# Optimization experiments

Measured on AMD Instinct MI355X. Metric: run time of the kernel, lower is better.

Reference implementation:

```python
import jax, jax.numpy as jnp
import numpy as np

B, D, R = 4096, 1024, 256
DT = 0.01
DT_SCALE = 1.0

# Yoshida 4th-order coefficients
_W1 = 1.0 / (2.0 - 2.0 ** (1.0 / 3.0))
_W0 = -(2.0 ** (1.0 / 3.0)) / (2.0 - 2.0 ** (1.0 / 3.0))
C1 = _W1 / 2.0
C2 = (_W0 + _W1) / 2.0
C3 = C2
C4 = C1
D1 = _W1
D2 = _W0
D3 = _W1


def setup_inputs() -> dict:
    key = jax.random.key(0)
    k1, k2, k3, k4, k5 = jax.random.split(key, 5)
    x = jax.random.normal(k1, (B, D), dtype=jnp.float32)
    v = jax.random.normal(k2, (B, D), dtype=jnp.float32)
    force = jax.random.normal(k3, (B, D), dtype=jnp.float32)
    # low-rank christoffel factors, scaled for numerical stability
    U = jax.random.normal(k4, (R, D), dtype=jnp.float32) * (1.0 / np.sqrt(D))
    W = jax.random.normal(k5, (D, R), dtype=jnp.float32) * (1.0 / np.sqrt(R))
    return {"x": x, "v": v, "force": force, "U": U, "W": W}


def _christoffel(tv, tx, U, W):
    # Gamma(v) = W @ (U v)^2  (low-rank quadratic form; x unused, matching
    # the gfn yoshida_fused(U, W) signature)
    h = jnp.einsum("rd,bd->br", U, tv)  # [B, R]
    return jnp.einsum("dr,br->bd", W, h * h)  # [B, D]


def reference(x, v, force, U, W):
    dt = DT * DT_SCALE

    def acceleration(tx, tv):
        return -_christoffel(tv, tx, U, W) + force

    x1 = x + C1 * dt * v
    v1 = v + D1 * dt * acceleration(x1, v)
    x2 = x1 + C2 * dt * v1
    v2 = v1 + D2 * dt * acceleration(x2, v1)
    x3 = x2 + C3 * dt * v2
    v3 = v2 + D3 * dt * acceleration(x3, v2)
    x_final = x3 + C4 * dt * v3
    return (x_final, v3)
```

## Files before the change

### kernel.cpp

```cpp
#include <hip/hip_runtime.h>
#include <hip/hip_bf16.h>


#define BSZ 4096
#define DD 1024
#define RR 256

typedef unsigned short ushort_t;
typedef __attribute__((ext_vector_type(8))) short short8;
typedef __attribute__((ext_vector_type(4))) float f32x4;

__device__ inline ushort_t f2b(float x) {
    union { float f; unsigned int u; } c;
    c.f = x;
    unsigned int lsb = (c.u >> 16) & 1u;
    return (ushort_t)((c.u + 0x7fffu + lsb) >> 16);
}

__global__ __launch_bounds__(256) void pack_uw_kernel(
    const float* __restrict__ U, const float* __restrict__ W,
    ushort_t* __restrict__ Upk, ushort_t* __restrict__ Wpk)
{
    const int g = blockIdx.x * 256 + threadIdx.x;
    if (g < 32768) {
        const int l = g & 63;
        const int kt = (g >> 6) & 31, nt = g >> 11;
        const int r = nt * 16 + (l & 15);
        const int d = kt * 32 + (l >> 4) * 8;
        const float* src = U + (size_t)r * DD + d;
        ushort_t* dst = Upk + (size_t)g * 8;
        #pragma unroll
        for (int j = 0; j < 8; ++j) dst[j] = f2b(src[j]);
    } else {
        const int g2 = g - 32768;
        const int l = g2 & 63;
        const int kt = (g2 >> 6) & 7, dtile = g2 >> 9;
        const int d = dtile * 16 + (l & 15);
        const int r = kt * 32 + (l >> 4) * 8;
        const float* src = W + (size_t)d * RR + r;
        ushort_t* dst = Wpk + (size_t)g2 * 8;
        #pragma unroll
        for (int j = 0; j < 8; ++j) dst[j] = f2b(src[j]);
    }
}

__global__ __launch_bounds__(1024) void yoshida_fused_kernel(
    const float* __restrict__ x_in,
    const float* __restrict__ v_in,
    const float* __restrict__ force,
    const ushort_t* __restrict__ Upk,
    const ushort_t* __restrict__ Wpk,
    float* __restrict__ x_out,
    float* __restrict__ v_out)
{
    __shared__ __align__(16) ushort_t vS[16][1032];
    __shared__ __align__(16) ushort_t H2S[16][264];

    const int tid = threadIdx.x;
    const int w = tid >> 6;
    const int l = tid & 63;
    const int m = l & 15;
    const int q = l >> 4;
    const int b0 = blockIdx.x * 16;
    const int d0 = w * 64;

    constexpr double CBRT2 = 1.2599210498948731647672106072782;
    constexpr double W1c = 1.0 / (2.0 - CBRT2);
    constexpr double W0c = -CBRT2 * W1c;
    constexpr double DTd = 0.01 * 1.0;
    const float dcoef[3] = {(float)(W1c * DTd), (float)(W0c * DTd), (float)(W1c * DTd)};
    const float xcoef[3] = {(float)((W0c + W1c) * 0.5), (float)((W0c + W1c) * 0.5),
                            (float)(W1c * 0.5)};
    const float c1  = (float)(W1c * 0.5);
    const float dtf = (float)DTd;

    {
        const int row = tid >> 6;
        const int col = (tid & 63) * 16;
        const float* src = v_in + (size_t)(b0 + row) * DD + col;
        ushort_t tmp[16];
        #pragma unroll
        for (int j = 0; j < 16; ++j) tmp[j] = f2b(src[j]);
        *(short8*)&vS[row][col]     = *(short8*)&tmp[0];
        *(short8*)&vS[row][col + 8] = *(short8*)&tmp[8];
    }

    float vreg[16], xacc[16];
    #pragma unroll
    for (int t = 0; t < 4; ++t)
        #pragma unroll
        for (int i = 0; i < 4; ++i) {
            const int row = q * 4 + i, col = d0 + t * 16 + m;
            const float vv = v_in[(size_t)(b0 + row) * DD + col];
            vreg[t * 4 + i] = vv;
            xacc[t * 4 + i] = c1 * vv;
        }
    __syncthreads();

    for (int s = 0; s < 3; ++s) {
        f32x4 accA = {0.f, 0.f, 0.f, 0.f};
        const ushort_t* up = Upk + (size_t)(w * 16384 + l * 8);
        #pragma unroll 4
        for (int kt = 0; kt < 32; ++kt) {
            short8 a = *(const short8*)&vS[m][kt * 32 + q * 8];
            short8 b = *(const short8*)(up + (size_t)kt * 512);
            accA = __builtin_amdgcn_mfma_f32_16x16x32_bf16(a, b, accA, 0, 0, 0);
        }
        #pragma unroll
        for (int i = 0; i < 4; ++i) {
            const float h = accA[i];
            H2S[q * 4 + i][w * 16 + m] = f2b(h * h);
        }
        __syncthreads();

        f32x4 accB[4];
        #pragma unroll
        for (int t = 0; t < 4; ++t) accB[t] = (f32x4){0.f, 0.f, 0.f, 0.f};
        const ushort_t* wp = Wpk + (size_t)(w * 16384 + l * 8);
        #pragma unroll 2
        for (int kt = 0; kt < 8; ++kt) {
            short8 a = *(const short8*)&H2S[m][kt * 32 + q * 8];
            #pragma unroll
            for (int t = 0; t < 4; ++t) {
                short8 b = *(const short8*)(wp + (size_t)(t * 8 + kt) * 512);
                accB[t] = __builtin_amdgcn_mfma_f32_16x16x32_bf16(a, b, accB[t], 0, 0, 0);
            }
        }

        const float ddt = dcoef[s], cx = xcoef[s];
        #pragma unroll
        for (int t = 0; t < 4; ++t)
            #pragma unroll
            for (int i = 0; i < 4; ++i) {
                const int row = q * 4 + i, col = d0 + t * 16 + m;
                const float fo = force[(size_t)(b0 + row) * DD + col];
                const float vn = vreg[t * 4 + i] + ddt * (fo - accB[t][i]);
                vreg[t * 4 + i] = vn;
                xacc[t * 4 + i] += cx * vn;
                vS[row][col] = f2b(vn);
            }
        __syncthreads();
    }

    #pragma unroll
    for (int t = 0; t < 4; ++t)
        #pragma unroll
        for (int i = 0; i < 4; ++i) {
            const int row = q * 4 + i, col = d0 + t * 16 + m;
            const size_t g = (size_t)(b0 + row) * DD + col;
            x_out[g] = x_in[g] + dtf * xacc[t * 4 + i];
            v_out[g] = vreg[t * 4 + i];
        }
}

extern "C" void kernel_launch(void* const* d_in, const int* in_sizes, int n_in,
                              void* d_out, int out_size, void* d_ws, size_t ws_size,
                              hipStream_t stream) {
    const float* x     = (const float*)d_in[0];
    const float* v     = (const float*)d_in[1];
    const float* force = (const float*)d_in[2];
    const float* U     = (const float*)d_in[3];
    const float* W     = (const float*)d_in[4];

    float* x_out = (float*)d_out;
    float* v_out = x_out + (size_t)BSZ * DD;

    ushort_t* Upk = (ushort_t*)d_ws;
    ushort_t* Wpk = Upk + (size_t)RR * DD;

    pack_uw_kernel<<<dim3(256), dim3(256), 0, stream>>>(U, W, Upk, Wpk);
    yoshida_fused_kernel<<<dim3(BSZ / 16), dim3(1024), 0, stream>>>(
        x, v, force, Upk, Wpk, x_out, v_out);
}
```

Baseline: 138.0 us.

## Software-pipeline U/W fragment loads, preload force, and vectorize conversions

The U and W bf16 fragments are now prefetched into registers several k-steps ahead in both MFMA loops, the stage loop is fully unrolled, and the first GEMM alternates between two accumulators to shorten the MFMA dependency chain. Force values are loaded once into registers at kernel start instead of being reloaded every stage, and the fp32 loads in the pack kernel and the initial v staging use float4 vector loads. The aim is to hide global-memory latency behind MFMA work and cut redundant traffic, at the cost of higher register pressure in a 1024-thread block.

```diff
diff --git a/kernel.cpp b/kernel.cpp
--- a/kernel.cpp
+++ b/kernel.cpp
@@ -22,26 +22,25 @@
     ushort_t* __restrict__ Upk, ushort_t* __restrict__ Wpk)
 {
     const int g = blockIdx.x * 256 + threadIdx.x;
+    const float* src;
+    ushort_t* dst;
     if (g < 32768) {
         const int l = g & 63;
         const int kt = (g >> 6) & 31, nt = g >> 11;
-        const int r = nt * 16 + (l & 15);
-        const int d = kt * 32 + (l >> 4) * 8;
-        const float* src = U + (size_t)r * DD + d;
-        ushort_t* dst = Upk + (size_t)g * 8;
-        #pragma unroll
-        for (int j = 0; j < 8; ++j) dst[j] = f2b(src[j]);
+        src = U + (size_t)(nt * 16 + (l & 15)) * DD + kt * 32 + (l >> 4) * 8;
+        dst = Upk + (size_t)g * 8;
     } else {
         const int g2 = g - 32768;
         const int l = g2 & 63;
         const int kt = (g2 >> 6) & 7, dtile = g2 >> 9;
-        const int d = dtile * 16 + (l & 15);
-        const int r = kt * 32 + (l >> 4) * 8;
-        const float* src = W + (size_t)d * RR + r;
-        ushort_t* dst = Wpk + (size_t)g2 * 8;
-        #pragma unroll
-        for (int j = 0; j < 8; ++j) dst[j] = f2b(src[j]);
+        src = W + (size_t)(dtile * 16 + (l & 15)) * RR + kt * 32 + (l >> 4) * 8;
+        dst = Wpk + (size_t)g2 * 8;
     }
+    const float4 a = *reinterpret_cast<const float4*>(src);
+    const float4 b = *reinterpret_cast<const float4*>(src + 4);
+    ushort_t t[8] = {f2b(a.x), f2b(a.y), f2b(a.z), f2b(a.w),
+                     f2b(b.x), f2b(b.y), f2b(b.z), f2b(b.w)};
+    *reinterpret_cast<short8*>(dst) = *reinterpret_cast<short8*>(t);
 }
 
 __global__ __launch_bounds__(1024) void yoshida_fused_kernel(
@@ -74,55 +73,79 @@
     const float c1  = (float)(W1c * 0.5);
     const float dtf = (float)DTd;
 
-    {
-        const int row = tid >> 6;
-        const int col = (tid & 63) * 16;
-        const float* src = v_in + (size_t)(b0 + row) * DD + col;
-        ushort_t tmp[16];
-        #pragma unroll
-        for (int j = 0; j < 16; ++j) tmp[j] = f2b(src[j]);
-        *(short8*)&vS[row][col]     = *(short8*)&tmp[0];
-        *(short8*)&vS[row][col + 8] = *(short8*)&tmp[8];
-    }
-
-    float vreg[16], xacc[16];
+    float vreg[16], xacc[16], freg[16];
     #pragma unroll
     for (int t = 0; t < 4; ++t)
         #pragma unroll
         for (int i = 0; i < 4; ++i) {
-            const int row = q * 4 + i, col = d0 + t * 16 + m;
-            const float vv = v_in[(size_t)(b0 + row) * DD + col];
+            const size_t gidx = (size_t)(b0 + q * 4 + i) * DD + d0 + t * 16 + m;
+            const float vv = v_in[gidx];
             vreg[t * 4 + i] = vv;
             xacc[t * 4 + i] = c1 * vv;
+            freg[t * 4 + i] = force[gidx];
         }
-    __syncthreads();
 
+    {
+        const int row = tid >> 6;
+        const int col = (tid & 63) * 16;
+        const float* sp = v_in + (size_t)(b0 + row) * DD + col;
+        const float4 f0 = *reinterpret_cast<const float4*>(sp);
+        const float4 f1 = *reinterpret_cast<const float4*>(sp + 4);
+        const float4 f2 = *reinterpret_cast<const float4*>(sp + 8);
+        const float4 f3 = *reinterpret_cast<const float4*>(sp + 12);
+        ushort_t tmp[16] = {f2b(f0.x), f2b(f0.y), f2b(f0.z), f2b(f0.w),
+                            f2b(f1.x), f2b(f1.y), f2b(f1.z), f2b(f1.w),
+                            f2b(f2.x), f2b(f2.y), f2b(f2.z), f2b(f2.w),
+                            f2b(f3.x), f2b(f3.y), f2b(f3.z), f2b(f3.w)};
+        *reinterpret_cast<short8*>(&vS[row][col])     = *reinterpret_cast<short8*>(&tmp[0]);
+        *reinterpret_cast<short8*>(&vS[row][col + 8]) = *reinterpret_cast<short8*>(&tmp[8]);
+    }
+
+    const ushort_t* up = Upk + (size_t)(w * 16384 + l * 8);
+    const ushort_t* wp = Wpk + (size_t)(w * 16384 + l * 8);
+
+    short8 ub[4];
+    #pragma unroll
+    for (int p = 0; p < 4; ++p)
+        ub[p] = *reinterpret_cast<const short8*>(up + (size_t)p * 512);
+
+    #pragma unroll
     for (int s = 0; s < 3; ++s) {
-        f32x4 accA = {0.f, 0.f, 0.f, 0.f};
-        const ushort_t* up = Upk + (size_t)(w * 16384 + l * 8);
-        #pragma unroll 4
+        __syncthreads();
+
+        f32x4 a0 = {0.f, 0.f, 0.f, 0.f}, a1 = {0.f, 0.f, 0.f, 0.f};
+        #pragma unroll
         for (int kt = 0; kt < 32; ++kt) {
-            short8 a = *(const short8*)&vS[m][kt * 32 + q * 8];
-            short8 b = *(const short8*)(up + (size_t)kt * 512);
-            accA = __builtin_amdgcn_mfma_f32_16x16x32_bf16(a, b, accA, 0, 0, 0);
+            const short8 b = ub[kt & 3];
+            if (kt < 28)
+                ub[kt & 3] = *reinterpret_cast<const short8*>(up + (size_t)(kt + 4) * 512);
+            const short8 a = *reinterpret_cast<const short8*>(&vS[m][kt * 32 + q * 8]);
+            if (kt & 1) a1 = __builtin_amdgcn_mfma_f32_16x16x32_bf16(a, b, a1, 0, 0, 0);
+            else        a0 = __builtin_amdgcn_mfma_f32_16x16x32_bf16(a, b, a0, 0, 0, 0);
         }
         #pragma unroll
         for (int i = 0; i < 4; ++i) {
-            const float h = accA[i];
+            const float h = a0[i] + a1[i];
             H2S[q * 4 + i][w * 16 + m] = f2b(h * h);
         }
+
+        short8 wb[4];
+        #pragma unroll
+        for (int t = 0; t < 4; ++t)
+            wb[t] = *reinterpret_cast<const short8*>(wp + (size_t)(t * 8) * 512);
         __syncthreads();
 
         f32x4 accB[4];
         #pragma unroll
         for (int t = 0; t < 4; ++t) accB[t] = (f32x4){0.f, 0.f, 0.f, 0.f};
-        const ushort_t* wp = Wpk + (size_t)(w * 16384 + l * 8);
-        #pragma unroll 2
+        #pragma unroll
         for (int kt = 0; kt < 8; ++kt) {
-            short8 a = *(const short8*)&H2S[m][kt * 32 + q * 8];
+            const short8 a = *reinterpret_cast<const short8*>(&H2S[m][kt * 32 + q * 8]);
             #pragma unroll
             for (int t = 0; t < 4; ++t) {
-                short8 b = *(const short8*)(wp + (size_t)(t * 8 + kt) * 512);
+                const short8 b = wb[t];
+                if (kt < 7)
+                    wb[t] = *reinterpret_cast<const short8*>(wp + (size_t)(t * 8 + kt + 1) * 512);
                 accB[t] = __builtin_amdgcn_mfma_f32_16x16x32_bf16(a, b, accB[t], 0, 0, 0);
             }
         }
@@ -132,22 +155,24 @@
         for (int t = 0; t < 4; ++t)
             #pragma unroll
             for (int i = 0; i < 4; ++i) {
-                const int row = q * 4 + i, col = d0 + t * 16 + m;
-                const float fo = force[(size_t)(b0 + row) * DD + col];
-                const float vn = vreg[t * 4 + i] + ddt * (fo - accB[t][i]);
+                const float vn = vreg[t * 4 + i] + ddt * (freg[t * 4 + i] - accB[t][i]);
                 vreg[t * 4 + i] = vn;
                 xacc[t * 4 + i] += cx * vn;
-                vS[row][col] = f2b(vn);
+                vS[q * 4 + i][d0 + t * 16 + m] = f2b(vn);
             }
-        __syncthreads();
+
+        if (s < 2) {
+            #pragma unroll
+            for (int p = 0; p < 4; ++p)
+                ub[p] = *reinterpret_cast<const short8*>(up + (size_t)p * 512);
+        }
     }
 
     #pragma unroll
     for (int t = 0; t < 4; ++t)
         #pragma unroll
         for (int i = 0; i < 4; ++i) {
-            const int row = q * 4 + i, col = d0 + t * 16 + m;
-            const size_t g = (size_t)(b0 + row) * DD + col;
+            const size_t g = (size_t)(b0 + q * 4 + i) * DD + d0 + t * 16 + m;
             x_out[g] = x_in[g] + dtf * xacc[t * 4 + i];
             v_out[g] = vreg[t * 4 + i];
         }
```

New measurement: 137.9 us. About the same (-0.0%).
